# Kernel optimization log

Hardware: AMD Instinct MI355X
Metric: run time of the kernel (lower is better)

## Reference

```python
import jax, jax.numpy as jnp
import numpy as np

GAMMA = 0.2
P = 3
N = 16384


def setup_inputs() -> dict:
    key = jax.random.key(0)
    k1, k2 = jax.random.split(key)
    y_pred = jax.random.normal(k1, (N, 2), dtype=jnp.float32)
    y_true = jax.random.randint(k2, (N,), 0, 2, dtype=jnp.int32)
    return {"y_pred": y_pred, "y_true": y_true}


def reference(y_pred, y_true):
    # softmax over classes, take probability of class 1 -> [N]
    s = jax.nn.softmax(y_pred, axis=-1)[:, 1]
    pos_mask = (y_true == 1)
    neg_mask = ~pos_mask
    # difference[j, i] = pos_i - neg_j - gamma  (rows: negatives, cols: positives)
    diff = s[None, :] - s[:, None] - GAMMA  # [N, N]
    pair = neg_mask[:, None] & pos_mask[None, :]
    valid = pair & (diff < 0.0)
    # sum of (-diff)^p over masked entries == hinge^p penalty
    contrib = jnp.where(valid, (-diff) ** P, jnp.zeros_like(diff))
    return jnp.sum(contrib)
```

## Files before the change

kernel.cpp:

```cpp
#include <hip/hip_runtime.h>
#include <math.h>

#define GAMMA_F 0.2f
#define NTHREADS 256
#define TILE 2048
#define NSPLIT 16

__device__ __forceinline__ float sigmoid_from_logits(float y0, float y1) {
    return 1.0f / (1.0f + __expf(y0 - y1));
}

__device__ __forceinline__ void block_reduce_and_atomic(float acc, float* out) {
    #pragma unroll
    for (int off = 32; off > 0; off >>= 1) acc += __shfl_down(acc, off, 64);
    __shared__ float wsum[NTHREADS / 64];
    int tid = threadIdx.x;
    int wave = tid >> 6, lane = tid & 63;
    if (lane == 0) wsum[wave] = acc;
    __syncthreads();
    if (tid == 0) {
        float s = 0.0f;
        #pragma unroll
        for (int w = 0; w < NTHREADS / 64; ++w) s += wsum[w];
        atomicAdd(out, s);
    }
}

__global__ void compact_kernel(const float* __restrict__ y_pred,
                               const int* __restrict__ y_true,
                               int n, int* __restrict__ counters,
                               float* __restrict__ pos_arr,
                               float* __restrict__ neg_arr) {
    int i = blockIdx.x * blockDim.x + threadIdx.x;
    bool valid = (i < n);
    bool is_pos = false;
    float s = 0.0f;
    if (valid) {
        float2 y = ((const float2*)y_pred)[i];
        s = sigmoid_from_logits(y.x, y.y);
        is_pos = (y_true[i] == 1);
    }
    unsigned long long mpos = __ballot(valid && is_pos);
    unsigned long long mneg = __ballot(valid && !is_pos);
    int lane = threadIdx.x & 63;
    unsigned long long lt = (1ULL << lane) - 1ULL;
    int base_pos = 0, base_neg = 0;
    if (lane == 0) {
        base_pos = atomicAdd(&counters[0], __popcll(mpos));
        base_neg = atomicAdd(&counters[1], __popcll(mneg));
    }
    base_pos = __shfl(base_pos, 0, 64);
    base_neg = __shfl(base_neg, 0, 64);
    if (valid) {
        if (is_pos) pos_arr[base_pos + __popcll(mpos & lt)] = s;
        else        neg_arr[base_neg + __popcll(mneg & lt)] = s;
    }
}

__global__ __launch_bounds__(NTHREADS) void pair_kernel(
        const int* __restrict__ counters,
        const float* __restrict__ pos_arr,
        const float* __restrict__ neg_arr,
        float* __restrict__ out) {
    __shared__ float lds[TILE];
    int n_pos = counters[0];
    int n_neg = counters[1];
    int base = blockIdx.x * NTHREADS;
    if (base >= n_pos) return;
    int tid = threadIdx.x;
    int i = base + tid;
    float aShift = (i < n_pos) ? (pos_arr[i] - GAMMA_F) : 1e30f;

    int len = (n_neg + NSPLIT - 1) / NSPLIT;
    int j0 = blockIdx.y * len;
    int j1 = min(n_neg, j0 + len);

    float acc0 = 0.0f, acc1 = 0.0f, acc2 = 0.0f, acc3 = 0.0f;
    for (int t0 = j0; t0 < j1; t0 += TILE) {
        int cnt = min(TILE, j1 - t0);
        __syncthreads();
        for (int k = tid; k < cnt; k += NTHREADS) lds[k] = neg_arr[t0 + k];
        __syncthreads();
        int cnt4 = cnt & ~3;
        const float4* lds4 = (const float4*)lds;
        for (int k4 = 0; k4 < (cnt4 >> 2); ++k4) {
            float4 b = lds4[k4];
            float t0f = fmaxf(b.x - aShift, 0.0f);
            float t1f = fmaxf(b.y - aShift, 0.0f);
            float t2f = fmaxf(b.z - aShift, 0.0f);
            float t3f = fmaxf(b.w - aShift, 0.0f);
            acc0 += t0f * t0f * t0f;
            acc1 += t1f * t1f * t1f;
            acc2 += t2f * t2f * t2f;
            acc3 += t3f * t3f * t3f;
        }
        for (int k = cnt4; k < cnt; ++k) {
            float t = fmaxf(lds[k] - aShift, 0.0f);
            acc0 += t * t * t;
        }
    }
    block_reduce_and_atomic((acc0 + acc1) + (acc2 + acc3), out);
}

__global__ __launch_bounds__(NTHREADS) void fused_kernel(
        const float* __restrict__ y_pred, const int* __restrict__ y_true,
        int n, float* __restrict__ out) {
    __shared__ float lds[TILE];
    int tid = threadIdx.x;
    int i = blockIdx.x * NTHREADS + tid;
    float aShift = 1e30f;
    if (i < n && y_true[i] == 1)
        aShift = sigmoid_from_logits(y_pred[2 * i], y_pred[2 * i + 1]) - GAMMA_F;

    int len = (n + NSPLIT - 1) / NSPLIT;
    int j0 = blockIdx.y * len;
    int j1 = min(n, j0 + len);

    float acc0 = 0.0f, acc1 = 0.0f, acc2 = 0.0f, acc3 = 0.0f;
    for (int t0 = j0; t0 < j1; t0 += TILE) {
        int cnt = min(TILE, j1 - t0);
        __syncthreads();
        for (int k = tid; k < cnt; k += NTHREADS) {
            int j = t0 + k;
            float b = -1e30f;
            if (y_true[j] != 1)
                b = sigmoid_from_logits(y_pred[2 * j], y_pred[2 * j + 1]);
            lds[k] = b;
        }
        __syncthreads();
        int cnt4 = cnt & ~3;
        const float4* lds4 = (const float4*)lds;
        for (int k4 = 0; k4 < (cnt4 >> 2); ++k4) {
            float4 b = lds4[k4];
            float t0f = fmaxf(b.x - aShift, 0.0f);
            float t1f = fmaxf(b.y - aShift, 0.0f);
            float t2f = fmaxf(b.z - aShift, 0.0f);
            float t3f = fmaxf(b.w - aShift, 0.0f);
            acc0 += t0f * t0f * t0f;
            acc1 += t1f * t1f * t1f;
            acc2 += t2f * t2f * t2f;
            acc3 += t3f * t3f * t3f;
        }
        for (int k = cnt4; k < cnt; ++k) {
            float t = fmaxf(lds[k] - aShift, 0.0f);
            acc0 += t * t * t;
        }
    }
    block_reduce_and_atomic((acc0 + acc1) + (acc2 + acc3), out);
}

extern "C" void kernel_launch(void* const* d_in, const int* in_sizes, int n_in,
                              void* d_out, int out_size, void* d_ws, size_t ws_size,
                              hipStream_t stream) {
    const float* y_pred = (const float*)d_in[0];
    const int* y_true = (const int*)d_in[1];
    int n = in_sizes[1];
    float* out = (float*)d_out;

    hipMemsetAsync(d_out, 0, sizeof(float), stream);

    size_t need = 16 * sizeof(int) + 2 * (size_t)n * sizeof(float);
    if (ws_size >= need) {
        int* counters = (int*)d_ws;
        float* pos_arr = (float*)d_ws + 16;
        float* neg_arr = pos_arr + n;
        hipMemsetAsync(d_ws, 0, 2 * sizeof(int), stream);
        int grid_a = (n + NTHREADS - 1) / NTHREADS;
        compact_kernel<<<grid_a, NTHREADS, 0, stream>>>(y_pred, y_true, n,
                                                        counters, pos_arr, neg_arr);
        dim3 grid_b((n + NTHREADS - 1) / NTHREADS, NSPLIT);
        pair_kernel<<<grid_b, NTHREADS, 0, stream>>>(counters, pos_arr, neg_arr, out);
    } else {
        dim3 grid((n + NTHREADS - 1) / NTHREADS, NSPLIT);
        fused_kernel<<<grid, NTHREADS, 0, stream>>>(y_pred, y_true, n, out);
    }
}
```

Baseline: 79.32 us.

## Fuse compaction into pair kernel with per-block LDS compaction and partials reduce

Replaces the separate global compaction kernel and pair kernel with one kernel. Each block compacts its own positive rows and its negative column slice into LDS, then does the dense pair loop over only those entries. Two threads share each row, each covering half of the columns. Per-block results go to a partials array that a small second kernel reduces, which removes the memsets and global atomics. The cost is that every block recomputes sigmoids for its column slice, and the grid is much larger (16 split chunks of 1024 columns).

Measured after the change: 70.73 us. 10.8% less time.

```diff
diff --git a/kernel.cpp b/kernel.cpp
--- a/kernel.cpp
+++ b/kernel.cpp
@@ -2,151 +2,126 @@
 #include <math.h>
 
 #define GAMMA_F 0.2f
-#define NTHREADS 256
-#define TILE 2048
-#define NSPLIT 16
+#define NT 256
+#define MAXLEN 1024
 
 __device__ __forceinline__ float sigmoid_from_logits(float y0, float y1) {
     return 1.0f / (1.0f + __expf(y0 - y1));
 }
 
-__device__ __forceinline__ void block_reduce_and_atomic(float acc, float* out) {
+__global__ __launch_bounds__(NT) void fused_pair_kernel(
+        const float* __restrict__ y_pred, const int* __restrict__ y_true,
+        int n, int len, float* __restrict__ partials) {
+    __shared__ float row_a[NT];
+    __shared__ float col_s[MAXLEN + 4];
+    __shared__ int cnts[2];
+    __shared__ float wsum[NT / 64];
+
+    int tid = threadIdx.x;
+    int lane = tid & 63;
+    unsigned long long lt = (1ULL << lane) - 1ULL;
+    if (tid < 2) cnts[tid] = 0;
+    __syncthreads();
+
+    {
+        int i = blockIdx.x * NT + tid;
+        bool in = (i < n);
+        float a = 0.0f;
+        bool is_pos = false;
+        if (in) {
+            float2 y = ((const float2*)y_pred)[i];
+            a = sigmoid_from_logits(y.x, y.y) - GAMMA_F;
+            is_pos = (y_true[i] == 1);
+        }
+        unsigned long long m = __ballot(is_pos);
+        int base = 0;
+        if (lane == 0) base = atomicAdd(&cnts[0], __popcll(m));
+        base = __shfl(base, 0, 64);
+        if (is_pos) row_a[base + __popcll(m & lt)] = a;
+    }
+
+    int j0 = blockIdx.y * len;
+    int j1 = min(n, j0 + len);
+    for (int c = j0; c < j1; c += NT) {
+        int j = c + tid;
+        bool in = (j < j1);
+        float s = 0.0f;
+        bool is_neg = false;
+        if (in) {
+            float2 y = ((const float2*)y_pred)[j];
+            s = sigmoid_from_logits(y.x, y.y);
+            is_neg = (y_true[j] != 1);
+        }
+        unsigned long long m = __ballot(is_neg);
+        int base = 0;
+        if (lane == 0) base = atomicAdd(&cnts[1], __popcll(m));
+        base = __shfl(base, 0, 64);
+        if (is_neg) col_s[base + __popcll(m & lt)] = s;
+    }
+    __syncthreads();
+
+    int n_rows = cnts[0];
+    int n_cols = cnts[1];
+
+    int half = (n_cols / 2) & ~3;
+    int p = tid & 1;
+    int c0 = p ? half : 0;
+    int c1 = p ? n_cols : half;
+    int c4len = (c1 - c0) & ~3;
+
+    float acc0 = 0.0f, acc1 = 0.0f, acc2 = 0.0f, acc3 = 0.0f;
+    for (int r = tid >> 1; r < n_rows; r += NT / 2) {
+        float av = row_a[r];
+        int c = c0;
+        int c4end = c0 + c4len;
+        for (; c < c4end; c += 4) {
+            float4 b = *(const float4*)&col_s[c];
+            float t0 = fmaxf(b.x - av, 0.0f);
+            float t1 = fmaxf(b.y - av, 0.0f);
+            float t2 = fmaxf(b.z - av, 0.0f);
+            float t3 = fmaxf(b.w - av, 0.0f);
+            acc0 += (t0 * t0) * t0;
+            acc1 += (t1 * t1) * t1;
+            acc2 += (t2 * t2) * t2;
+            acc3 += (t3 * t3) * t3;
+        }
+        for (; c < c1; ++c) {
+            float t = fmaxf(col_s[c] - av, 0.0f);
+            acc0 += (t * t) * t;
+        }
+    }
+    float acc = (acc0 + acc1) + (acc2 + acc3);
+
     #pragma unroll
     for (int off = 32; off > 0; off >>= 1) acc += __shfl_down(acc, off, 64);
-    __shared__ float wsum[NTHREADS / 64];
-    int tid = threadIdx.x;
-    int wave = tid >> 6, lane = tid & 63;
+    int wave = tid >> 6;
     if (lane == 0) wsum[wave] = acc;
     __syncthreads();
     if (tid == 0) {
         float s = 0.0f;
         #pragma unroll
-        for (int w = 0; w < NTHREADS / 64; ++w) s += wsum[w];
-        atomicAdd(out, s);
+        for (int w = 0; w < NT / 64; ++w) s += wsum[w];
+        partials[blockIdx.y * gridDim.x + blockIdx.x] = s;
     }
 }
 
-__global__ void compact_kernel(const float* __restrict__ y_pred,
-                               const int* __restrict__ y_true,
-                               int n, int* __restrict__ counters,
-                               float* __restrict__ pos_arr,
-                               float* __restrict__ neg_arr) {
-    int i = blockIdx.x * blockDim.x + threadIdx.x;
-    bool valid = (i < n);
-    bool is_pos = false;
+__global__ __launch_bounds__(NT) void reduce_kernel(
+        const float* __restrict__ partials, int nb, float* __restrict__ out) {
+    int tid = threadIdx.x;
     float s = 0.0f;
-    if (valid) {
-        float2 y = ((const float2*)y_pred)[i];
-        s = sigmoid_from_logits(y.x, y.y);
-        is_pos = (y_true[i] == 1);
+    for (int k = tid; k < nb; k += NT) s += partials[k];
+    #pragma unroll
+    for (int off = 32; off > 0; off >>= 1) s += __shfl_down(s, off, 64);
+    __shared__ float wsum[NT / 64];
+    int wave = tid >> 6, lane = tid & 63;
+    if (lane == 0) wsum[wave] = s;
+    __syncthreads();
+    if (tid == 0) {
+        float t = 0.0f;
+        #pragma unroll
+        for (int w = 0; w < NT / 64; ++w) t += wsum[w];
+        out[0] = t;
     }
-    unsigned long long mpos = __ballot(valid && is_pos);
-    unsigned long long mneg = __ballot(valid && !is_pos);
-    int lane = threadIdx.x & 63;
-    unsigned long long lt = (1ULL << lane) - 1ULL;
-    int base_pos = 0, base_neg = 0;
-    if (lane == 0) {
-        base_pos = atomicAdd(&counters[0], __popcll(mpos));
-        base_neg = atomicAdd(&counters[1], __popcll(mneg));
-    }
-    base_pos = __shfl(base_pos, 0, 64);
-    base_neg = __shfl(base_neg, 0, 64);
-    if (valid) {
-        if (is_pos) pos_arr[base_pos + __popcll(mpos & lt)] = s;
-        else        neg_arr[base_neg + __popcll(mneg & lt)] = s;
-    }
-}
-
-__global__ __launch_bounds__(NTHREADS) void pair_kernel(
-        const int* __restrict__ counters,
-        const float* __restrict__ pos_arr,
-        const float* __restrict__ neg_arr,
-        float* __restrict__ out) {
-    __shared__ float lds[TILE];
-    int n_pos = counters[0];
-    int n_neg = counters[1];
-    int base = blockIdx.x * NTHREADS;
-    if (base >= n_pos) return;
-    int tid = threadIdx.x;
-    int i = base + tid;
-    float aShift = (i < n_pos) ? (pos_arr[i] - GAMMA_F) : 1e30f;
-
-    int len = (n_neg + NSPLIT - 1) / NSPLIT;
-    int j0 = blockIdx.y * len;
-    int j1 = min(n_neg, j0 + len);
-
-    float acc0 = 0.0f, acc1 = 0.0f, acc2 = 0.0f, acc3 = 0.0f;
-    for (int t0 = j0; t0 < j1; t0 += TILE) {
-        int cnt = min(TILE, j1 - t0);
-        __syncthreads();
-        for (int k = tid; k < cnt; k += NTHREADS) lds[k] = neg_arr[t0 + k];
-        __syncthreads();
-        int cnt4 = cnt & ~3;
-        const float4* lds4 = (const float4*)lds;
-        for (int k4 = 0; k4 < (cnt4 >> 2); ++k4) {
-            float4 b = lds4[k4];
-            float t0f = fmaxf(b.x - aShift, 0.0f);
-            float t1f = fmaxf(b.y - aShift, 0.0f);
-            float t2f = fmaxf(b.z - aShift, 0.0f);
-            float t3f = fmaxf(b.w - aShift, 0.0f);
-            acc0 += t0f * t0f * t0f;
-            acc1 += t1f * t1f * t1f;
-            acc2 += t2f * t2f * t2f;
-            acc3 += t3f * t3f * t3f;
-        }
-        for (int k = cnt4; k < cnt; ++k) {
-            float t = fmaxf(lds[k] - aShift, 0.0f);
-            acc0 += t * t * t;
-        }
-    }
-    block_reduce_and_atomic((acc0 + acc1) + (acc2 + acc3), out);
-}
-
-__global__ __launch_bounds__(NTHREADS) void fused_kernel(
-        const float* __restrict__ y_pred, const int* __restrict__ y_true,
-        int n, float* __restrict__ out) {
-    __shared__ float lds[TILE];
-    int tid = threadIdx.x;
-    int i = blockIdx.x * NTHREADS + tid;
-    float aShift = 1e30f;
-    if (i < n && y_true[i] == 1)
-        aShift = sigmoid_from_logits(y_pred[2 * i], y_pred[2 * i + 1]) - GAMMA_F;
-
-    int len = (n + NSPLIT - 1) / NSPLIT;
-    int j0 = blockIdx.y * len;
-    int j1 = min(n, j0 + len);
-
-    float acc0 = 0.0f, acc1 = 0.0f, acc2 = 0.0f, acc3 = 0.0f;
-    for (int t0 = j0; t0 < j1; t0 += TILE) {
-        int cnt = min(TILE, j1 - t0);
-        __syncthreads();
-        for (int k = tid; k < cnt; k += NTHREADS) {
-            int j = t0 + k;
-            float b = -1e30f;
-            if (y_true[j] != 1)
-                b = sigmoid_from_logits(y_pred[2 * j], y_pred[2 * j + 1]);
-            lds[k] = b;
-        }
-        __syncthreads();
-        int cnt4 = cnt & ~3;
-        const float4* lds4 = (const float4*)lds;
-        for (int k4 = 0; k4 < (cnt4 >> 2); ++k4) {
-            float4 b = lds4[k4];
-            float t0f = fmaxf(b.x - aShift, 0.0f);
-            float t1f = fmaxf(b.y - aShift, 0.0f);
-            float t2f = fmaxf(b.z - aShift, 0.0f);
-            float t3f = fmaxf(b.w - aShift, 0.0f);
-            acc0 += t0f * t0f * t0f;
-            acc1 += t1f * t1f * t1f;
-            acc2 += t2f * t2f * t2f;
-            acc3 += t3f * t3f * t3f;
-        }
-        for (int k = cnt4; k < cnt; ++k) {
-            float t = fmaxf(lds[k] - aShift, 0.0f);
-            acc0 += t * t * t;
-        }
-    }
-    block_reduce_and_atomic((acc0 + acc1) + (acc2 + acc3), out);
 }
 
 extern "C" void kernel_launch(void* const* d_in, const int* in_sizes, int n_in,
@@ -157,21 +132,14 @@
     int n = in_sizes[1];
     float* out = (float*)d_out;
 
-    hipMemsetAsync(d_out, 0, sizeof(float), stream);
+    int gx = (n + NT - 1) / NT;
+    int nsplit = (n + MAXLEN - 1) / MAXLEN;
+    int len = (n + nsplit - 1) / nsplit;
+    int nb = gx * nsplit;
 
-    size_t need = 16 * sizeof(int) + 2 * (size_t)n * sizeof(float);
-    if (ws_size >= need) {
-        int* counters = (int*)d_ws;
-        float* pos_arr = (float*)d_ws + 16;
-        float* neg_arr = pos_arr + n;
-        hipMemsetAsync(d_ws, 0, 2 * sizeof(int), stream);
-        int grid_a = (n + NTHREADS - 1) / NTHREADS;
-        compact_kernel<<<grid_a, NTHREADS, 0, stream>>>(y_pred, y_true, n,
-                                                        counters, pos_arr, neg_arr);
-        dim3 grid_b((n + NTHREADS - 1) / NTHREADS, NSPLIT);
-        pair_kernel<<<grid_b, NTHREADS, 0, stream>>>(counters, pos_arr, neg_arr, out);
-    } else {
-        dim3 grid((n + NTHREADS - 1) / NTHREADS, NSPLIT);
-        fused_kernel<<<grid, NTHREADS, 0, stream>>>(y_pred, y_true, n, out);
-    }
+    float* partials = (float*)d_ws;
+
+    dim3 grid(gx, nsplit);
+    fused_pair_kernel<<<grid, NT, 0, stream>>>(y_pred, y_true, n, len, partials);
+    reduce_kernel<<<1, NT, 0, stream>>>(partials, nb, out);
 }
```
